# Optimization experiments

Hardware: AMD Instinct MI355X
Metric: run time of the kernel (lower is better)

## Reference

```python
import jax, jax.numpy as jnp
import numpy as np

BOND_TOL = 0.4
CLASH_TOL = 1.5
IDEAL_CA_CA = 3.8
EPS = 1e-08


def setup_inputs() -> dict:
    key = jax.random.key(0)
    k1, _ = jax.random.split(key)
    B, L = 8, 2048
    positions = jax.random.normal(k1, (B, L, 3), dtype=jnp.float32) * 10.0
    mask = jnp.ones((B, L), dtype=jnp.float32)
    return {"positions": positions, "mask": mask}


def reference(positions, mask):
    # positions: [B, L, 3] CA coordinates; mask: [B, L]
    L = positions.shape[1]
    ca = positions
    ca_mask = mask

    # --- bond term: consecutive CA-CA distances ---
    ca_diff = ca[:, 1:] - ca[:, :-1]                       # [B, L-1, 3]
    ca_dist = jnp.sqrt(jnp.sum(ca_diff ** 2, axis=-1) + EPS)
    bond_violation = jax.nn.relu(jnp.abs(ca_dist - IDEAL_CA_CA) - BOND_TOL)
    bond_mask = ca_mask[:, 1:] * ca_mask[:, :-1]
    bond_loss = jnp.sum(bond_violation * bond_mask) / (jnp.sum(bond_mask) + EPS)

    # --- clash term: all-pairs distances, non-bonded (|i-j| > 2) ---
    all_diff = ca[:, :, None, :] - ca[:, None, :, :]       # [B, L, L, 3]
    all_dist = jnp.sqrt(jnp.sum(all_diff ** 2, axis=-1) + EPS)  # [B, L, L]
    idx = jnp.arange(L)
    seq_sep = jnp.abs(idx[None, :] - idx[:, None])         # [L, L]
    non_bonded = (seq_sep > 2).astype(ca.dtype)
    clash_violation = jax.nn.relu(CLASH_TOL - all_dist)
    pair_mask = ca_mask[:, :, None] * ca_mask[:, None, :] * non_bonded[None]
    clash_loss = jnp.sum(clash_violation * pair_mask) / (jnp.sum(pair_mask) + EPS)

    total = bond_loss + clash_loss
    # stacked: [bond_loss, clash_loss, total_violation]
    return jnp.stack([bond_loss, clash_loss, total])
```

## Files before the change

### kernel.cpp

```cpp
#include <hip/hip_runtime.h>

#define TPB 512
#define RPB 16
#define SEQ_L 2048
#define CHUNK 512
#define NCH (SEQ_L / CHUNK)
#define NBATCH 8
#define NPAIR 64
#define NBLOCKS (NBATCH * NPAIR)
#define NWAVE (TPB / 64)

static constexpr float kBondTol  = 0.4f;
static constexpr float kClashTol = 1.5f;
static constexpr float kIdeal    = 3.8f;
static constexpr float kEps      = 1e-8f;
static constexpr float kThresh2  = 2.25f;

__device__ __forceinline__ float wred(float v) {
#pragma unroll
  for (int o = 32; o > 0; o >>= 1) v += __shfl_down(v, o, 64);
  return v;
}

__global__ __launch_bounds__(TPB, 4) void viol_main(
    const float* __restrict__ pos,
    const float* __restrict__ mask,
    float4* __restrict__ partial) {
  __shared__ float4 s[SEQ_L];
  __shared__ float  redm[NWAVE];
  __shared__ float  red4[NWAVE][4];

  const int b  = blockIdx.x & 7;
  const int g  = blockIdx.x >> 3;
  const int i0A = g << 4;
  const int i0B = (127 - g) << 4;
  const int k0A = i0A >> 9;
  const int k0B = i0B >> 9;
  const int jbase = k0A << 9;

  const float* pb = pos  + (size_t)b * SEQ_L * 3;
  const float* mb = mask + (size_t)b * SEQ_L;

  float mpart = 0.f;
#pragma unroll
  for (int it = 0; it < NCH; ++it) mpart += mb[threadIdx.x + (it << 9)];
  mpart = wred(mpart);

  for (int idx = jbase + (int)threadIdx.x; idx < SEQ_L; idx += TPB) {
    float x = pb[3 * idx + 0];
    float y = pb[3 * idx + 1];
    float z = pb[3 * idx + 2];
    s[idx] = make_float4(x, y, z, mb[idx]);
  }

  const int wid  = threadIdx.x >> 6;
  const int lane = threadIdx.x & 63;
  if (lane == 0) redm[wid] = mpart;
  __syncthreads();
  float msum = 0.f;
#pragma unroll
  for (int w = 0; w < NWAVE; ++w) msum += redm[w];

  float cv = 0.f, pm = 0.f, bv = 0.f, bm = 0.f;

#pragma unroll
  for (int tt = 0; tt < 2; ++tt) {
    const int i0 = tt ? i0B : i0A;
    const int k0 = tt ? k0B : k0A;

    float px[RPB], py[RPB], pz[RPB], pw[RPB], accr[RPB];
#pragma unroll
    for (int q = 0; q < RPB; ++q) {
      float4 p = s[i0 + q];
      px[q] = p.x; py[q] = p.y; pz[q] = p.z; pw[q] = p.w;
      accr[q] = 0.f;
    }

    {
      const int j = (int)threadIdx.x + (k0 << 9);
      const float4 pj = s[j];
#pragma unroll
      for (int q = 0; q < RPB; ++q) {
        const int i = i0 + q;
        float dx = pj.x - px[q];
        float dy = pj.y - py[q];
        float dz = pj.z - pz[q];
        float d2 = fmaf(dx, dx, fmaf(dy, dy, dz * dz));
        float dist = __builtin_amdgcn_sqrtf(d2 + kEps);
        float mw = (j > i) ? pj.w : 0.f;
        accr[q] = fmaf(fmaxf(kClashTol - dist, 0.f), mw, accr[q]);
      }
    }

    for (int k = k0 + 1; k < NCH; ++k) {
      float4 pj = s[threadIdx.x + (k << 9)];
      float d2r[RPB];
#pragma unroll
      for (int q = 0; q < RPB; ++q) {
        float dx = pj.x - px[q];
        float dy = pj.y - py[q];
        float dz = pj.z - pz[q];
        d2r[q] = fmaf(dx, dx, fmaf(dy, dy, dz * dz));
      }
      float mv = d2r[0];
#pragma unroll
      for (int q = 1; q < RPB; ++q) mv = fminf(mv, d2r[q]);
      if (__ballot(mv < kThresh2) != 0ull) {
#pragma unroll
        for (int q = 0; q < RPB; ++q) {
          float dist = __builtin_amdgcn_sqrtf(d2r[q] + kEps);
          accr[q] = fmaf(fmaxf(kClashTol - dist, 0.f), pj.w, accr[q]);
        }
      }
    }

#pragma unroll
    for (int q = 0; q < RPB; ++q) cv = fmaf(pw[q], accr[q], cv);
  }

  if (threadIdx.x < 32) {
    const int i = ((threadIdx.x & 16) ? i0B : i0A) + (int)(threadIdx.x & 15);
    const float4 pi = s[i];
    float nv = 0.f;
    const int jhi = (i + 2 > SEQ_L - 1) ? SEQ_L - 1 : i + 2;
    for (int j = i + 1; j <= jhi; ++j) {
      float4 pj = s[j];
      float dx = pj.x - pi.x;
      float dy = pj.y - pi.y;
      float dz = pj.z - pi.z;
      float dist = __builtin_amdgcn_sqrtf(dx * dx + dy * dy + dz * dz + kEps);
      nv += fmaxf(kClashTol - dist, 0.f) * pj.w;
    }
    cv -= pi.w * nv;

    float nm = 0.f;
    const int jlo = (i - 2 < 0) ? 0 : i - 2;
    for (int j = jlo; j <= jhi; ++j) nm += mb[j];
    pm += pi.w * (msum - nm);

    if (i < SEQ_L - 1) {
      const float4 pj = s[i + 1];
      float dx = pj.x - pi.x;
      float dy = pj.y - pi.y;
      float dz = pj.z - pi.z;
      float dist = __builtin_amdgcn_sqrtf(dx * dx + dy * dy + dz * dz + kEps);
      float viol = fmaxf(fabsf(dist - kIdeal) - kBondTol, 0.f);
      bv += viol * pi.w * pj.w;
      bm += pi.w * pj.w;
    }
  }

  bv = wred(bv); bm = wred(bm); cv = wred(cv); pm = wred(pm);
  if (lane == 0) {
    red4[wid][0] = bv; red4[wid][1] = bm;
    red4[wid][2] = cv; red4[wid][3] = pm;
  }
  __syncthreads();
  if (threadIdx.x == 0) {
    float tbv = 0.f, tbm = 0.f, tcv = 0.f, tpm = 0.f;
#pragma unroll
    for (int w = 0; w < NWAVE; ++w) {
      tbv += red4[w][0]; tbm += red4[w][1];
      tcv += red4[w][2]; tpm += red4[w][3];
    }
    partial[blockIdx.x] = make_float4(tbv, tbm, 2.f * tcv, tpm);
  }
}

__global__ __launch_bounds__(256) void viol_reduce(
    const float4* __restrict__ partial, float* __restrict__ out) {
  __shared__ float red4[4][4];
  float bv = 0.f, bm = 0.f, cv = 0.f, pm = 0.f;
#pragma unroll
  for (int i = threadIdx.x; i < NBLOCKS; i += 256) {
    float4 p = partial[i];
    bv += p.x; bm += p.y; cv += p.z; pm += p.w;
  }
  bv = wred(bv); bm = wred(bm); cv = wred(cv); pm = wred(pm);
  const int wid  = threadIdx.x >> 6;
  const int lane = threadIdx.x & 63;
  if (lane == 0) {
    red4[wid][0] = bv; red4[wid][1] = bm;
    red4[wid][2] = cv; red4[wid][3] = pm;
  }
  __syncthreads();
  if (threadIdx.x == 0) {
    float tbv = 0.f, tbm = 0.f, tcv = 0.f, tpm = 0.f;
#pragma unroll
    for (int w = 0; w < 4; ++w) {
      tbv += red4[w][0]; tbm += red4[w][1];
      tcv += red4[w][2]; tpm += red4[w][3];
    }
    float bond  = tbv / (tbm + kEps);
    float clash = tcv / (tpm + kEps);
    out[0] = bond;
    out[1] = clash;
    out[2] = bond + clash;
  }
}

extern "C" void kernel_launch(void* const* d_in, const int* in_sizes, int n_in,
                              void* d_out, int out_size, void* d_ws, size_t ws_size,
                              hipStream_t stream) {
  const float* pos  = (const float*)d_in[0];
  const float* mask = (const float*)d_in[1];
  float* out = (float*)d_out;
  float4* partial = (float4*)d_ws;

  viol_main<<<dim3(NBLOCKS), dim3(TPB), 0, stream>>>(pos, mask, partial);
  viol_reduce<<<dim3(1), dim3(256), 0, stream>>>(partial, out);
}
```

Measured before the change: 73.29 us.

## Halve block size and rows per block, doubling grid with full shared staging

Switches to 256-thread blocks with 8 rows per tile and 256-wide chunks, doubling the number of blocks to 1024. Every block now stages the whole sequence into shared memory, folds the mask sum into that staging pass, and reads the neighbour mask from shared memory instead of global. The aim is more blocks and finer-grained early-exit ballots for better load balance. The cost is redundant staging loads per block and less register reuse per loaded j point.

```diff
diff --git a/kernel.cpp b/kernel.cpp
--- a/kernel.cpp
+++ b/kernel.cpp
@@ -1,12 +1,12 @@
 #include <hip/hip_runtime.h>
 
-#define TPB 512
-#define RPB 16
+#define TPB 256
+#define RPB 8
 #define SEQ_L 2048
-#define CHUNK 512
+#define CHUNK 256
 #define NCH (SEQ_L / CHUNK)
 #define NBATCH 8
-#define NPAIR 64
+#define NPAIR 128
 #define NBLOCKS (NBATCH * NPAIR)
 #define NWAVE (TPB / 64)
 
@@ -30,40 +30,36 @@
   __shared__ float  redm[NWAVE];
   __shared__ float  red4[NWAVE][4];
 
-  const int b  = blockIdx.x & 7;
-  const int g  = blockIdx.x >> 3;
-  const int i0A = g << 4;
-  const int i0B = (127 - g) << 4;
-  const int k0A = i0A >> 9;
-  const int k0B = i0B >> 9;
-  const int jbase = k0A << 9;
+  const int b = blockIdx.x & 7;
+  const int t = blockIdx.x >> 3;
+  const int i0A = t << 3;
+  const int i0B = (255 - t) << 3;
+  const int k0A = i0A >> 8;
+  const int k0B = i0B >> 8;
 
   const float* pb = pos  + (size_t)b * SEQ_L * 3;
   const float* mb = mask + (size_t)b * SEQ_L;
 
   float mpart = 0.f;
 #pragma unroll
-  for (int it = 0; it < NCH; ++it) mpart += mb[threadIdx.x + (it << 9)];
-  mpart = wred(mpart);
-
-  for (int idx = jbase + (int)threadIdx.x; idx < SEQ_L; idx += TPB) {
+  for (int it = 0; it < NCH; ++it) {
+    int idx = (int)threadIdx.x + (it << 8);
     float x = pb[3 * idx + 0];
     float y = pb[3 * idx + 1];
     float z = pb[3 * idx + 2];
-    s[idx] = make_float4(x, y, z, mb[idx]);
-  }
-
+    float m = mb[idx];
+    s[idx] = make_float4(x, y, z, m);
+    mpart += m;
+  }
+  mpart = wred(mpart);
   const int wid  = threadIdx.x >> 6;
   const int lane = threadIdx.x & 63;
   if (lane == 0) redm[wid] = mpart;
   __syncthreads();
-  float msum = 0.f;
-#pragma unroll
-  for (int w = 0; w < NWAVE; ++w) msum += redm[w];
+  const float msum = redm[0] + redm[1] + redm[2] + redm[3];
 
   float cv = 0.f, pm = 0.f, bv = 0.f, bm = 0.f;
 
-#pragma unroll
   for (int tt = 0; tt < 2; ++tt) {
     const int i0 = tt ? i0B : i0A;
     const int k0 = tt ? k0B : k0A;
@@ -77,7 +73,7 @@
     }
 
     {
-      const int j = (int)threadIdx.x + (k0 << 9);
+      const int j = (int)threadIdx.x + (k0 << 8);
       const float4 pj = s[j];
 #pragma unroll
       for (int q = 0; q < RPB; ++q) {
@@ -92,8 +88,9 @@
       }
     }
 
+#pragma unroll 2
     for (int k = k0 + 1; k < NCH; ++k) {
-      float4 pj = s[threadIdx.x + (k << 9)];
+      float4 pj = s[threadIdx.x + (k << 8)];
       float d2r[RPB];
 #pragma unroll
       for (int q = 0; q < RPB; ++q) {
@@ -118,8 +115,8 @@
     for (int q = 0; q < RPB; ++q) cv = fmaf(pw[q], accr[q], cv);
   }
 
-  if (threadIdx.x < 32) {
-    const int i = ((threadIdx.x & 16) ? i0B : i0A) + (int)(threadIdx.x & 15);
+  if (threadIdx.x < 16) {
+    const int i = ((threadIdx.x & 8) ? i0B : i0A) + (int)(threadIdx.x & 7);
     const float4 pi = s[i];
     float nv = 0.f;
     const int jhi = (i + 2 > SEQ_L - 1) ? SEQ_L - 1 : i + 2;
@@ -135,7 +132,7 @@
 
     float nm = 0.f;
     const int jlo = (i - 2 < 0) ? 0 : i - 2;
-    for (int j = jlo; j <= jhi; ++j) nm += mb[j];
+    for (int j = jlo; j <= jhi; ++j) nm += s[j].w;
     pm += pi.w * (msum - nm);
 
     if (i < SEQ_L - 1) {
@@ -167,12 +164,12 @@
   }
 }
 
-__global__ __launch_bounds__(256) void viol_reduce(
+__global__ __launch_bounds__(TPB) void viol_reduce(
     const float4* __restrict__ partial, float* __restrict__ out) {
-  __shared__ float red4[4][4];
+  __shared__ float red4[NWAVE][4];
   float bv = 0.f, bm = 0.f, cv = 0.f, pm = 0.f;
 #pragma unroll
-  for (int i = threadIdx.x; i < NBLOCKS; i += 256) {
+  for (int i = threadIdx.x; i < NBLOCKS; i += TPB) {
     float4 p = partial[i];
     bv += p.x; bm += p.y; cv += p.z; pm += p.w;
   }
@@ -187,7 +184,7 @@
   if (threadIdx.x == 0) {
     float tbv = 0.f, tbm = 0.f, tcv = 0.f, tpm = 0.f;
 #pragma unroll
-    for (int w = 0; w < 4; ++w) {
+    for (int w = 0; w < NWAVE; ++w) {
       tbv += red4[w][0]; tbm += red4[w][1];
       tcv += red4[w][2]; tpm += red4[w][3];
     }
@@ -208,5 +205,5 @@
   float4* partial = (float4*)d_ws;
 
   viol_main<<<dim3(NBLOCKS), dim3(TPB), 0, stream>>>(pos, mask, partial);
-  viol_reduce<<<dim3(1), dim3(256), 0, stream>>>(partial, out);
-}
+  viol_reduce<<<dim3(1), dim3(TPB), 0, stream>>>(partial, out);
+}
```

Result: faster. 63.86 us (-12.9%).
